# Kernel optimization log

Hardware: AMD Instinct MI355X
Metric: run time of the kernel (lower is better)

Reference implementation:

```python
import jax, jax.numpy as jnp
import numpy as np

HEAD_DIM = 64
AGGR = 4  # attn_aggr_ratio
BN_EPS = 1e-5


def _conv1x1(x, W, b=None):
    # x: [N, Cin, L], W: [Cout, Cin] -> [N, Cout, L]
    y = jnp.einsum('ncl,oc->nol', x, W)
    if b is not None:
        y = y + b[None, :, None]
    return y


def _bn(x, gamma, beta, mean, var):
    # BatchNorm1d, eval mode (running stats). x: [N, C, L]
    inv = gamma * jax.lax.rsqrt(var + BN_EPS)
    return x * inv[None, :, None] + (beta - mean * inv)[None, :, None]


def setup_inputs() -> dict:
    key = jax.random.key(0)
    ks = jax.random.split(key, 8)
    N, C, L = 4, 256, 4096
    s = 1.0 / np.sqrt(C)
    inp = {
        'x': jax.random.normal(ks[0], (N, C, L), jnp.float32),
        'Wq': jax.random.normal(ks[1], (C, C), jnp.float32) * s,
        'bq': jnp.zeros((C,), jnp.float32),
        'Wk': jax.random.normal(ks[2], (C, C), jnp.float32) * s,
        'bk': jnp.zeros((C,), jnp.float32),
        'Wv': jax.random.normal(ks[3], (C, C), jnp.float32) * s,
        'bv': jnp.zeros((C,), jnp.float32),
        'Wo': jax.random.normal(ks[4], (C, C), jnp.float32) * s,
        'bo': jnp.zeros((C,), jnp.float32),
        'Wa': jax.random.normal(ks[5], (C, C), jnp.float32) * s,
        'g1': jnp.ones((C,), jnp.float32), 'b1': jnp.zeros((C,), jnp.float32),
        'm1': jnp.zeros((C,), jnp.float32), 'v1': jnp.ones((C,), jnp.float32),
        'g2': jnp.ones((C,), jnp.float32), 'b2': jnp.zeros((C,), jnp.float32),
        'm2': jnp.zeros((C,), jnp.float32), 'v2': jnp.ones((C,), jnp.float32),
    }
    return inp


def reference(x, Wq, bq, Wk, bk, Wv, bv, Wo, bo, Wa,
              g1, b1, m1, v1, g2, b2, m2, v2):
    N, C, L = x.shape
    H, E = C // HEAD_DIM, HEAD_DIM
    # q projection on full-resolution input
    q = _conv1x1(x, Wq, bq).reshape(N, H, E, L)
    # LocalAwareAggregationBlock: avg+max pool (kernel=AGGR, L divisible), 1x1 conv, BN
    xp = x.reshape(N, C, L // AGGR, AGGR)
    xa = xp.mean(axis=-1) + xp.max(axis=-1)          # [N, C, L//AGGR]
    xa = _conv1x1(xa, Wa)                             # bias=False
    xa = _bn(xa, g1, b1, m1, v1)
    # post-aggregation norm
    xa = _bn(xa, g2, b2, m2, v2)
    k = _conv1x1(xa, Wk, bk).reshape(N, H, E, -1)     # [N, H, E, L2]
    v = _conv1x1(xa, Wv, bv).reshape(N, H, E, -1)
    # attention: softmax((q/sqrt(E))^T k) @ v^T
    scale = 1.0 / np.sqrt(E)
    scores = jnp.einsum('nhel,nhem->nhlm', q * scale, k)  # [N, H, L, L2]
    attn = jax.nn.softmax(scores, axis=-1)
    o = jnp.einsum('nhlm,nhem->nhel', attn, v).reshape(N, C, L)
    return _conv1x1(o, Wo, bo)
```

## Files before the change

### kernel.cpp

```cpp
#include <hip/hip_runtime.h>
#include <stdint.h>

constexpr int NBATCH = 4;
constexpr int CH     = 256;
constexpr int LEN    = 4096;
constexpr int LPOOL  = 1024;
constexpr int NH     = 4;
constexpr int HD     = 64;

typedef __attribute__((ext_vector_type(8))) short short8;
typedef __attribute__((ext_vector_type(4))) float float4e;
typedef __attribute__((ext_vector_type(16))) float float16e;
typedef __attribute__((ext_vector_type(2))) unsigned uint2v;

__device__ __forceinline__ unsigned short f2bf(float f) {
    union { unsigned int i; float f; } v; v.f = f;
    unsigned int lsb = (v.i >> 16) & 1u;
    v.i += 0x7fffu + lsb;
    return (unsigned short)(v.i >> 16);
}
__device__ __forceinline__ unsigned pack2bf(float lo, float hi) {
    unsigned a = __float_as_uint(lo) + 0x8000u;
    unsigned b = __float_as_uint(hi) + 0x8000u;
    return __builtin_amdgcn_perm(b, a, 0x07060302u);
}
__device__ __forceinline__ float fast_exp2(float x) {
#if __has_builtin(__builtin_amdgcn_exp2f)
    return __builtin_amdgcn_exp2f(x);
#else
    float r;
    asm("v_exp_f32 %0, %1" : "=v"(r) : "v"(x));
    return r;
#endif
}

__global__ __launch_bounds__(256) void transpool_setup(
    const float* __restrict__ x, unsigned short* __restrict__ xbf,
    unsigned short* __restrict__ poolT,
    const float* __restrict__ w0, const float* __restrict__ w1,
    const float* __restrict__ w2, const float* __restrict__ w3,
    const float* __restrict__ w4, unsigned short* __restrict__ outW,
    const float* __restrict__ g1, const float* __restrict__ b1,
    const float* __restrict__ m1, const float* __restrict__ v1,
    const float* __restrict__ g2, const float* __restrict__ b2,
    const float* __restrict__ m2, const float* __restrict__ v2,
    float* __restrict__ scale, float* __restrict__ shift,
    const float* __restrict__ bk, const float* __restrict__ bv,
    float* __restrict__ bkv)
{
    __shared__ float T[64][65];
    __shared__ float P16[64][17];
    int b = blockIdx.x, t = threadIdx.x;
    if (b >= 1024) {
        int sb = b - 1024;
        if (sb < 320) {
            int gid = sb * 256 + t;
            int w = gid >> 14;
            int off = (gid & 16383) * 4;
            const float* src = (w == 0) ? w0 : (w == 1) ? w1 : (w == 2) ? w2 : (w == 3) ? w3 : w4;
            float4 v = *(const float4*)(src + off);
            uint2 pk;
            pk.x = pack2bf(v.x, v.y);
            pk.y = pack2bf(v.z, v.w);
            *(uint2*)(outW + w * 65536 + off) = pk;
        } else {
            float inv1 = g1[t] * rsqrtf(v1[t] + 1e-5f);
            float inv2 = g2[t] * rsqrtf(v2[t] + 1e-5f);
            scale[t] = inv1 * inv2;
            shift[t] = (b1[t] - m1[t] * inv1) * inv2 + (b2[t] - m2[t] * inv2);
            bkv[t] = bk[t];
            bkv[256 + t] = bv[t];
        }
        return;
    }
    int n = b >> 8, c0 = ((b >> 6) & 3) * 64, l0 = (b & 63) * 64;
    const float* xp = x + ((size_t)n * CH + c0) * LEN + l0;
    #pragma unroll
    for (int i = 0; i < 4; i++) {
        int idx = t + i * 256;
        int c = idx >> 4, l4 = idx & 15;
        float4 v = *(const float4*)(xp + (size_t)c * LEN + l4 * 4);
        T[c][l4 * 4 + 0] = v.x; T[c][l4 * 4 + 1] = v.y;
        T[c][l4 * 4 + 2] = v.z; T[c][l4 * 4 + 3] = v.w;
        P16[c][l4] = (v.x + v.y + v.z + v.w) * 0.25f
                   + fmaxf(fmaxf(v.x, v.y), fmaxf(v.z, v.w));
    }
    __syncthreads();
    unsigned short* op = xbf + ((size_t)n * LEN + l0) * CH + c0;
    #pragma unroll
    for (int i = 0; i < 4; i++) {
        int idx = t + i * 256;
        int l = idx >> 4, c4 = idx & 15;
        uint2 pk;
        pk.x = pack2bf(T[c4 * 4 + 0][l], T[c4 * 4 + 1][l]);
        pk.y = pack2bf(T[c4 * 4 + 2][l], T[c4 * 4 + 3][l]);
        *(uint2*)(op + (size_t)l * CH + c4 * 4) = pk;
    }
    int p0 = l0 >> 2;
    #pragma unroll
    for (int k = 0; k < 2; k++) {
        int p = (t >> 5) + k * 8;
        int c2 = (t & 31) * 2;
        unsigned pk = pack2bf(P16[c2][p], P16[c2 + 1][p]);
        *(unsigned*)(poolT + ((size_t)n * LPOOL + p0 + p) * CH + c0 + c2) = pk;
    }
}

__global__ __launch_bounds__(256) void gemm_mfma(
    const unsigned short* __restrict__ A,
    const unsigned short* __restrict__ B, size_t bBatch,
    const float* __restrict__ biasRow,
    const float* __restrict__ scale, const float* __restrict__ shift,
    float* __restrict__ outF, size_t oFBatch,
    unsigned short* __restrict__ out1, size_t o1Batch, int cs1,
    unsigned short* __restrict__ out2, size_t o2Batch, int rs2, int rowSplit,
    int NN, float outScale)
{
    __shared__ unsigned short smem[2 * 128 * 72];
    unsigned short* As = smem;
    unsigned short* Bs = smem + 128 * 72;

    int n = blockIdx.z;
    int t = threadIdx.x;
    int wave = t >> 6, lane = t & 63, m = lane & 15, quad = lane >> 4;
    int wm = wave & 1, wn = wave >> 1;
    int rowTile = blockIdx.y * 128;
    int col0 = blockIdx.x * 128;

    const unsigned short* Ab = A + (size_t)rowTile * 256;
    const unsigned short* Bb = B + (size_t)n * bBatch + (size_t)col0 * 256;

    float4e acc[4][4] = {};

    for (int kk = 0; kk < 256; kk += 64) {
        #pragma unroll
        for (int i = 0; i < 4; i++) {
            int idx = t + i * 256;
            int row = idx >> 3, ch = idx & 7;
            *(uint4*)&As[row * 72 + ch * 8] = *(const uint4*)(Ab + (size_t)row * 256 + kk + ch * 8);
            *(uint4*)&Bs[row * 72 + ch * 8] = *(const uint4*)(Bb + (size_t)row * 256 + kk + ch * 8);
        }
        __syncthreads();
        #pragma unroll
        for (int kc = 0; kc < 2; kc++) {
            short8 af[4], bfr[4];
            #pragma unroll
            for (int i = 0; i < 4; i++)
                af[i] = *(const short8*)&As[(wm * 64 + i * 16 + m) * 72 + kc * 32 + quad * 8];
            #pragma unroll
            for (int j = 0; j < 4; j++)
                bfr[j] = *(const short8*)&Bs[(wn * 64 + j * 16 + m) * 72 + kc * 32 + quad * 8];
            #pragma unroll
            for (int i = 0; i < 4; i++)
                #pragma unroll
                for (int j = 0; j < 4; j++)
                    acc[i][j] = __builtin_amdgcn_mfma_f32_16x16x32_bf16(af[i], bfr[j], acc[i][j], 0, 0, 0);
        }
        __syncthreads();
    }

    if (outF) {
        float* TOf = (float*)smem;
        float* dst = outF + (size_t)n * oFBatch;
        #pragma unroll
        for (int half = 0; half < 2; half++) {
            __syncthreads();
            if (wm == half) {
                #pragma unroll
                for (int i = 0; i < 4; i++) {
                    int rowL = i * 16 + quad * 4;
                    int rowG = rowTile + half * 64 + rowL;
                    float br[4], sc[4], sh[4];
                    #pragma unroll
                    for (int r = 0; r < 4; r++) {
                        br[r] = biasRow ? biasRow[rowG + r] : 0.0f;
                        sc[r] = scale ? scale[rowG + r] : 1.0f;
                        sh[r] = shift ? shift[rowG + r] : 0.0f;
                    }
                    #pragma unroll
                    for (int j = 0; j < 4; j++) {
                        int colL = wn * 64 + j * 16 + m;
                        float4e c = acc[i][j];
                        #pragma unroll
                        for (int r = 0; r < 4; r++)
                            TOf[(rowL + r) * 128 + colL] = ((c[r] + br[r]) * sc[r] + sh[r]) * outScale;
                    }
                }
            }
            __syncthreads();
            #pragma unroll
            for (int w = 0; w < 8; w++) {
                int idx = t + w * 256;
                int row = idx >> 5, c4 = idx & 31;
                *(float4*)(dst + (size_t)(rowTile + half * 64 + row) * NN + col0 + c4 * 4) =
                    *(const float4*)&TOf[row * 128 + c4 * 4];
            }
        }
        return;
    }

    bool mode2 = (rowTile >= rowSplit);
    unsigned short* TO = smem;
    #pragma unroll
    for (int i = 0; i < 4; i++) {
        int rowL = wm * 64 + i * 16 + quad * 4;
        int rowG = rowTile + rowL;
        float br[4], sc[4], sh[4];
        #pragma unroll
        for (int r = 0; r < 4; r++) {
            br[r] = biasRow ? biasRow[rowG + r] : 0.0f;
            sc[r] = scale ? scale[rowG + r] : 1.0f;
            sh[r] = shift ? shift[rowG + r] : 0.0f;
        }
        #pragma unroll
        for (int j = 0; j < 4; j++) {
            int colL = wn * 64 + j * 16 + m;
            float4e c = acc[i][j];
            float v0 = ((c[0] + br[0]) * sc[0] + sh[0]) * outScale;
            float v1 = ((c[1] + br[1]) * sc[1] + sh[1]) * outScale;
            float v2 = ((c[2] + br[2]) * sc[2] + sh[2]) * outScale;
            float v3 = ((c[3] + br[3]) * sc[3] + sh[3]) * outScale;
            if (!mode2) {
                uint2 pk;
                pk.x = pack2bf(v0, v1);
                pk.y = pack2bf(v2, v3);
                *(uint2*)&TO[colL * 136 + rowL] = pk;
            } else {
                TO[(rowL + 0) * 136 + colL] = f2bf(v0);
                TO[(rowL + 1) * 136 + colL] = f2bf(v1);
                TO[(rowL + 2) * 136 + colL] = f2bf(v2);
                TO[(rowL + 3) * 136 + colL] = f2bf(v3);
            }
        }
    }
    __syncthreads();
    if (!mode2) {
        unsigned short* dst = out1 + (size_t)n * o1Batch;
        #pragma unroll
        for (int w = 0; w < 8; w++) {
            int idx = t + w * 256;
            int l = idx >> 4, ch = idx & 15;
            *(uint4*)(dst + (size_t)(col0 + l) * cs1 + rowTile + ch * 8) =
                *(const uint4*)&TO[l * 136 + ch * 8];
        }
    } else {
        unsigned short* dst = out2 + (size_t)n * o2Batch;
        int rowBase = rowTile - rowSplit;
        #pragma unroll
        for (int w = 0; w < 8; w++) {
            int idx = t + w * 256;
            int row = idx >> 4, ch = idx & 15;
            *(uint4*)(dst + (size_t)(rowBase + row) * rs2 + col0 + ch * 8) =
                *(const uint4*)&TO[row * 136 + ch * 8];
        }
    }
}

__global__ __launch_bounds__(256, 2) void attn_mfma(
    const unsigned short* __restrict__ Qb,
    const unsigned short* __restrict__ Kb,
    const unsigned short* __restrict__ Vb,
    unsigned short* __restrict__ Obf)
{
    __shared__ unsigned short Ks[2][64 * 64];
    __shared__ unsigned short Vs[2][64 * 64];

    int qb = blockIdx.x;
    int h  = blockIdx.y;
    int n  = blockIdx.z;
    int t  = threadIdx.x;
    int wave = t >> 6, lane = t & 63;
    int col = lane & 31;
    int hi  = lane >> 5;
    int l0 = qb * 128 + wave * 32;

    const unsigned short* qp = Qb + ((size_t)n * LEN + l0 + col) * CH + h * HD + hi * 8;
    short8 bQ[4];
    #pragma unroll
    for (int dc = 0; dc < 4; dc++)
        bQ[dc] = *(const short8*)(qp + dc * 16);

    float16e Oa[2];
    #pragma unroll
    for (int e = 0; e < 2; e++)
        #pragma unroll
        for (int r = 0; r < 16; r++) Oa[e][r] = 0.0f;
    float l_run = 0.0f;

    const unsigned short* KgBase = Kb + (size_t)n * LPOOL * CH + h * HD;
    const unsigned short* VgBase = Vb + ((size_t)n * CH + h * HD) * LPOOL;
    const float NEG = -17.312340f;

    int srow[2], sch[2], sdst[2];
    #pragma unroll
    for (int i = 0; i < 2; i++) {
        int idx = t + i * 256;
        srow[i] = idx >> 3; sch[i] = idx & 7;
        sdst[i] = srow[i] * 128 + ((sch[i] * 16) ^ ((srow[i] & 7) << 4));
    }
    const unsigned short* kp[2];
    const unsigned short* vp[2];
    #pragma unroll
    for (int i = 0; i < 2; i++) {
        kp[i] = KgBase + (size_t)srow[i] * CH + sch[i] * 8;
        vp[i] = VgBase + (size_t)srow[i] * LPOOL + sch[i] * 8;
    }
    int ldoff[2][4];
    #pragma unroll
    for (int g = 0; g < 2; g++)
        #pragma unroll
        for (int c = 0; c < 4; c++) {
            int row = g * 32 + col;
            ldoff[g][c] = row * 128 + ((c * 32 + hi * 16) ^ ((row & 7) << 4));
        }

    uint4 kreg[2], vreg[2];
    #pragma unroll
    for (int i = 0; i < 2; i++) {
        kreg[i] = *(const uint4*)kp[i];
        vreg[i] = *(const uint4*)vp[i];
        kp[i] += 64 * CH;
        vp[i] += 64;
    }
    #pragma unroll
    for (int i = 0; i < 2; i++) {
        *(uint4*)((char*)Ks[0] + sdst[i]) = kreg[i];
        *(uint4*)((char*)Vs[0] + sdst[i]) = vreg[i];
    }
    __syncthreads();

    for (int kt = 0; kt < 16; kt++) {
        int cur = kt & 1;
        if (kt < 15) {
            #pragma unroll
            for (int i = 0; i < 2; i++) {
                kreg[i] = *(const uint4*)kp[i];
                vreg[i] = *(const uint4*)vp[i];
                kp[i] += 64 * CH;
                vp[i] += 64;
            }
        }

        const char* KsC = (const char*)Ks[cur];
        const char* VsC = (const char*)Vs[cur];
        #pragma unroll
        for (int kh = 0; kh < 2; kh++) {
            float16e c;
            #pragma unroll
            for (int r = 0; r < 16; r++) c[r] = NEG;
            __builtin_amdgcn_s_setprio(1);
            #pragma unroll
            for (int dc = 0; dc < 4; dc++) {
                short8 a = *(const short8*)(KsC + ldoff[kh][dc]);
                c = __builtin_amdgcn_mfma_f32_32x32x16_bf16(a, bQ[dc], c, 0, 0, 0);
            }
            __builtin_amdgcn_s_setprio(0);
            float p[16];
            #pragma unroll
            for (int r = 0; r < 16; r++) p[r] = fast_exp2(c[r]);
            l_run += ((p[0] + p[1]) + (p[2] + p[3])) + ((p[4] + p[5]) + (p[6] + p[7]))
                   + ((p[8] + p[9]) + (p[10] + p[11])) + ((p[12] + p[13]) + (p[14] + p[15]));
            union { unsigned u[4]; short8 s; } bP[2];
            #pragma unroll
            for (int kc2 = 0; kc2 < 2; kc2++) {
                int rb = kc2 * 8;
                unsigned A0 = pack2bf(p[rb + 0], p[rb + 1]);
                unsigned B0 = pack2bf(p[rb + 4], p[rb + 5]);
                unsigned A1 = pack2bf(p[rb + 2], p[rb + 3]);
                unsigned B1 = pack2bf(p[rb + 6], p[rb + 7]);
                uint2v s0 = __builtin_amdgcn_permlane32_swap(A0, B0, false, false);
                uint2v s1 = __builtin_amdgcn_permlane32_swap(A1, B1, false, false);
                bP[kc2].u[0] = s0[0];
                bP[kc2].u[1] = s1[0];
                bP[kc2].u[2] = s0[1];
                bP[kc2].u[3] = s1[1];
            }
            __builtin_amdgcn_s_setprio(1);
            #pragma unroll
            for (int eh = 0; eh < 2; eh++)
                #pragma unroll
                for (int kc2 = 0; kc2 < 2; kc2++) {
                    short8 av = *(const short8*)(VsC + ldoff[eh][kh * 2 + kc2]);
                    Oa[eh] = __builtin_amdgcn_mfma_f32_32x32x16_bf16(av, bP[kc2].s, Oa[eh], 0, 0, 0);
                }
            __builtin_amdgcn_s_setprio(0);
        }

        if (kt < 15) {
            int nxt = cur ^ 1;
            #pragma unroll
            for (int i = 0; i < 2; i++) {
                *(uint4*)((char*)Ks[nxt] + sdst[i]) = kreg[i];
                *(uint4*)((char*)Vs[nxt] + sdst[i]) = vreg[i];
            }
            __syncthreads();
        }
    }

    float l = l_run + __shfl_xor(l_run, 32);
    float inv = 1.0f / l;
    unsigned short* op = Obf + ((size_t)n * LEN + l0 + col) * CH + h * HD + hi * 4;
    #pragma unroll
    for (int eh = 0; eh < 2; eh++)
        #pragma unroll
        for (int rq = 0; rq < 4; rq++) {
            int r = rq * 4;
            uint2 pk;
            pk.x = pack2bf(Oa[eh][r + 0] * inv, Oa[eh][r + 1] * inv);
            pk.y = pack2bf(Oa[eh][r + 2] * inv, Oa[eh][r + 3] * inv);
            *(uint2*)(op + eh * 32 + rq * 8) = pk;
        }
}

extern "C" void kernel_launch(void* const* d_in, const int* in_sizes, int n_in,
                              void* d_out, int out_size, void* d_ws, size_t ws_size,
                              hipStream_t stream)
{
    const float* x  = (const float*)d_in[0];
    const float* Wq = (const float*)d_in[1];
    const float* bq = (const float*)d_in[2];
    const float* Wk = (const float*)d_in[3];
    const float* bk = (const float*)d_in[4];
    const float* Wv = (const float*)d_in[5];
    const float* bv = (const float*)d_in[6];
    const float* Wo = (const float*)d_in[7];
    const float* bo = (const float*)d_in[8];
    const float* Wa = (const float*)d_in[9];
    const float* g1 = (const float*)d_in[10];
    const float* b1 = (const float*)d_in[11];
    const float* m1 = (const float*)d_in[12];
    const float* v1 = (const float*)d_in[13];
    const float* g2 = (const float*)d_in[14];
    const float* b2 = (const float*)d_in[15];
    const float* m2 = (const float*)d_in[16];
    const float* v2 = (const float*)d_in[17];

    float* wsf      = (float*)d_ws;
    float* bn_scale = wsf;
    float* bn_shift = wsf + 256;
    float* bkv      = wsf + 512;
    unsigned short* Wbf   = (unsigned short*)(wsf + 1024);
    unsigned short* xbf   = Wbf + 5 * 65536;
    unsigned short* poolT = xbf   + (size_t)NBATCH * LEN * CH;
    unsigned short* xabf  = poolT + (size_t)NBATCH * LPOOL * CH;
    unsigned short* Kbf   = xabf  + (size_t)NBATCH * LPOOL * CH;
    unsigned short* Vbf   = Kbf   + (size_t)NBATCH * LPOOL * CH;
    unsigned short* Qbf   = Vbf   + (size_t)NBATCH * LPOOL * CH;
    unsigned short* Obf   = Qbf   + (size_t)NBATCH * LEN * CH;

    transpool_setup<<<1345, 256, 0, stream>>>(x, xbf, poolT,
        Wq, Wk, Wv, Wo, Wa, Wbf,
        g1, b1, m1, v1, g2, b2, m2, v2, bn_scale, bn_shift, bk, bv, bkv);

    gemm_mfma<<<dim3(32, 2, 4), 256, 0, stream>>>(
        Wbf + 0 * 65536, xbf, (size_t)LEN * CH, bq, nullptr, nullptr,
        nullptr, 0, Qbf, (size_t)LEN * CH, 256, nullptr, 0, 0, 1 << 30,
        LEN, 0.18033688f);

    gemm_mfma<<<dim3(8, 2, 4), 256, 0, stream>>>(
        Wbf + 4 * 65536, poolT, (size_t)LPOOL * CH, nullptr, bn_scale, bn_shift,
        nullptr, 0, xabf, (size_t)LPOOL * CH, 256, nullptr, 0, 0, 1 << 30,
        LPOOL, 1.0f);

    gemm_mfma<<<dim3(8, 4, 4), 256, 0, stream>>>(
        Wbf + 1 * 65536, xabf, (size_t)LPOOL * CH, bkv, nullptr, nullptr,
        nullptr, 0, Kbf, (size_t)LPOOL * CH, 256, Vbf, (size_t)LPOOL * CH, LPOOL, 256,
        LPOOL, 1.0f);

    attn_mfma<<<dim3(LEN / 128, NH, NBATCH), 256, 0, stream>>>(Qbf, Kbf, Vbf, Obf);

    gemm_mfma<<<dim3(32, 2, 4), 256, 0, stream>>>(
        Wbf + 3 * 65536, Obf, (size_t)LEN * CH, bo, nullptr, nullptr,
        (float*)d_out, (size_t)CH * LEN, nullptr, 0, 0, nullptr, 0, 0, 1 << 30,
        LEN, 1.0f);
}
```

Baseline: 182.0 us.

## Split attention keys across waves and read K/V fragments directly from global

The attention kernel now gives each block 64 queries instead of 128. Within a block, two pairs of waves each cover half of the 1024 pooled keys, and their partial outputs and softmax sums are combined through shared memory at the end. The double-buffered LDS staging of K/V tiles and the per-tile barriers are gone: each lane loads its MFMA fragments straight from global/L2 memory, and launch bounds are raised to allow more resident blocks. The aim is more parallelism and occupancy with fewer syncs, at the cost of more, less coalesced global loads, since each K/V fragment is now fetched by twice as many blocks.

```diff
diff --git a/kernel.cpp b/kernel.cpp
--- a/kernel.cpp
+++ b/kernel.cpp
@@ -256,14 +256,13 @@
     }
 }
 
-__global__ __launch_bounds__(256, 2) void attn_mfma(
+__global__ __launch_bounds__(256, 4) void attn_mfma(
     const unsigned short* __restrict__ Qb,
     const unsigned short* __restrict__ Kb,
     const unsigned short* __restrict__ Vb,
     unsigned short* __restrict__ Obf)
 {
-    __shared__ unsigned short Ks[2][64 * 64];
-    __shared__ unsigned short Vs[2][64 * 64];
+    __shared__ float comb[2 * 64 * 33];
 
     int qb = blockIdx.x;
     int h  = blockIdx.y;
@@ -272,7 +271,10 @@
     int wave = t >> 6, lane = t & 63;
     int col = lane & 31;
     int hi  = lane >> 5;
-    int l0 = qb * 128 + wave * 32;
+    int qc = wave & 1;
+    int ks = wave >> 1;
+    int l0 = qb * 64 + qc * 32;
+    int kbase = ks * 512;
 
     const unsigned short* qp = Qb + ((size_t)n * LEN + l0 + col) * CH + h * HD + hi * 8;
     short8 bQ[4];
@@ -287,129 +289,101 @@
         for (int r = 0; r < 16; r++) Oa[e][r] = 0.0f;
     float l_run = 0.0f;
 
-    const unsigned short* KgBase = Kb + (size_t)n * LPOOL * CH + h * HD;
-    const unsigned short* VgBase = Vb + ((size_t)n * CH + h * HD) * LPOOL;
     const float NEG = -17.312340f;
 
-    int srow[2], sch[2], sdst[2];
-    #pragma unroll
-    for (int i = 0; i < 2; i++) {
-        int idx = t + i * 256;
-        srow[i] = idx >> 3; sch[i] = idx & 7;
-        sdst[i] = srow[i] * 128 + ((sch[i] * 16) ^ ((srow[i] & 7) << 4));
-    }
-    const unsigned short* kp[2];
-    const unsigned short* vp[2];
-    #pragma unroll
-    for (int i = 0; i < 2; i++) {
-        kp[i] = KgBase + (size_t)srow[i] * CH + sch[i] * 8;
-        vp[i] = VgBase + (size_t)srow[i] * LPOOL + sch[i] * 8;
-    }
-    int ldoff[2][4];
-    #pragma unroll
-    for (int g = 0; g < 2; g++)
-        #pragma unroll
-        for (int c = 0; c < 4; c++) {
-            int row = g * 32 + col;
-            ldoff[g][c] = row * 128 + ((c * 32 + hi * 16) ^ ((row & 7) << 4));
-        }
-
-    uint4 kreg[2], vreg[2];
-    #pragma unroll
-    for (int i = 0; i < 2; i++) {
-        kreg[i] = *(const uint4*)kp[i];
-        vreg[i] = *(const uint4*)vp[i];
-        kp[i] += 64 * CH;
-        vp[i] += 64;
-    }
-    #pragma unroll
-    for (int i = 0; i < 2; i++) {
-        *(uint4*)((char*)Ks[0] + sdst[i]) = kreg[i];
-        *(uint4*)((char*)Vs[0] + sdst[i]) = vreg[i];
+    const unsigned short* kPtr =
+        Kb + ((size_t)n * LPOOL + kbase + col) * CH + h * HD + hi * 8;
+    const unsigned short* vPtr0 =
+        Vb + ((size_t)n * CH + h * HD + col) * LPOOL + kbase + hi * 8;
+    const unsigned short* vPtr1 = vPtr0 + (size_t)32 * LPOOL;
+
+    #pragma unroll 2
+    for (int kt = 0; kt < 16; kt++) {
+        short8 kf0 = *(const short8*)(kPtr);
+        short8 kf1 = *(const short8*)(kPtr + 16);
+        short8 kf2 = *(const short8*)(kPtr + 32);
+        short8 kf3 = *(const short8*)(kPtr + 48);
+        short8 av00 = *(const short8*)(vPtr0);
+        short8 av01 = *(const short8*)(vPtr0 + 16);
+        short8 av10 = *(const short8*)(vPtr1);
+        short8 av11 = *(const short8*)(vPtr1 + 16);
+        kPtr  += 32 * CH;
+        vPtr0 += 32;
+        vPtr1 += 32;
+
+        float16e c;
+        #pragma unroll
+        for (int r = 0; r < 16; r++) c[r] = NEG;
+        __builtin_amdgcn_s_setprio(1);
+        c = __builtin_amdgcn_mfma_f32_32x32x16_bf16(kf0, bQ[0], c, 0, 0, 0);
+        c = __builtin_amdgcn_mfma_f32_32x32x16_bf16(kf1, bQ[1], c, 0, 0, 0);
+        c = __builtin_amdgcn_mfma_f32_32x32x16_bf16(kf2, bQ[2], c, 0, 0, 0);
+        c = __builtin_amdgcn_mfma_f32_32x32x16_bf16(kf3, bQ[3], c, 0, 0, 0);
+        __builtin_amdgcn_s_setprio(0);
+
+        float p[16];
+        #pragma unroll
+        for (int r = 0; r < 16; r++) p[r] = fast_exp2(c[r]);
+        l_run += ((p[0] + p[1]) + (p[2] + p[3])) + ((p[4] + p[5]) + (p[6] + p[7]))
+               + ((p[8] + p[9]) + (p[10] + p[11])) + ((p[12] + p[13]) + (p[14] + p[15]));
+
+        union { unsigned u[4]; short8 s; } bP[2];
+        #pragma unroll
+        for (int kc2 = 0; kc2 < 2; kc2++) {
+            int rb = kc2 * 8;
+            unsigned A0 = pack2bf(p[rb + 0], p[rb + 1]);
+            unsigned B0 = pack2bf(p[rb + 4], p[rb + 5]);
+            unsigned A1 = pack2bf(p[rb + 2], p[rb + 3]);
+            unsigned B1 = pack2bf(p[rb + 6], p[rb + 7]);
+            uint2v s0 = __builtin_amdgcn_permlane32_swap(A0, B0, false, false);
+            uint2v s1 = __builtin_amdgcn_permlane32_swap(A1, B1, false, false);
+            bP[kc2].u[0] = s0[0];
+            bP[kc2].u[1] = s1[0];
+            bP[kc2].u[2] = s0[1];
+            bP[kc2].u[3] = s1[1];
+        }
+
+        __builtin_amdgcn_s_setprio(1);
+        Oa[0] = __builtin_amdgcn_mfma_f32_32x32x16_bf16(av00, bP[0].s, Oa[0], 0, 0, 0);
+        Oa[0] = __builtin_amdgcn_mfma_f32_32x32x16_bf16(av01, bP[1].s, Oa[0], 0, 0, 0);
+        Oa[1] = __builtin_amdgcn_mfma_f32_32x32x16_bf16(av10, bP[0].s, Oa[1], 0, 0, 0);
+        Oa[1] = __builtin_amdgcn_mfma_f32_32x32x16_bf16(av11, bP[1].s, Oa[1], 0, 0, 0);
+        __builtin_amdgcn_s_setprio(0);
+    }
+
+    if (wave >= 2) {
+        float* cb = &comb[((wave - 2) * 64 + lane) * 33];
+        #pragma unroll
+        for (int eh = 0; eh < 2; eh++)
+            #pragma unroll
+            for (int r = 0; r < 16; r++)
+                cb[eh * 16 + r] = Oa[eh][r];
+        cb[32] = l_run;
     }
     __syncthreads();
-
-    for (int kt = 0; kt < 16; kt++) {
-        int cur = kt & 1;
-        if (kt < 15) {
-            #pragma unroll
-            for (int i = 0; i < 2; i++) {
-                kreg[i] = *(const uint4*)kp[i];
-                vreg[i] = *(const uint4*)vp[i];
-                kp[i] += 64 * CH;
-                vp[i] += 64;
+    if (wave < 2) {
+        const float* cb = &comb[(wave * 64 + lane) * 33];
+        #pragma unroll
+        for (int eh = 0; eh < 2; eh++)
+            #pragma unroll
+            for (int r = 0; r < 16; r++)
+                Oa[eh][r] += cb[eh * 16 + r];
+        l_run += cb[32];
+
+        float l = l_run + __shfl_xor(l_run, 32);
+        float inv = 1.0f / l;
+        unsigned short* op = Obf + ((size_t)n * LEN + l0 + col) * CH + h * HD + hi * 4;
+        #pragma unroll
+        for (int eh = 0; eh < 2; eh++)
+            #pragma unroll
+            for (int rq = 0; rq < 4; rq++) {
+                int r = rq * 4;
+                uint2 pk;
+                pk.x = pack2bf(Oa[eh][r + 0] * inv, Oa[eh][r + 1] * inv);
+                pk.y = pack2bf(Oa[eh][r + 2] * inv, Oa[eh][r + 3] * inv);
+                *(uint2*)(op + eh * 32 + rq * 8) = pk;
             }
-        }
-
-        const char* KsC = (const char*)Ks[cur];
-        const char* VsC = (const char*)Vs[cur];
-        #pragma unroll
-        for (int kh = 0; kh < 2; kh++) {
-            float16e c;
-            #pragma unroll
-            for (int r = 0; r < 16; r++) c[r] = NEG;
-            __builtin_amdgcn_s_setprio(1);
-            #pragma unroll
-            for (int dc = 0; dc < 4; dc++) {
-                short8 a = *(const short8*)(KsC + ldoff[kh][dc]);
-                c = __builtin_amdgcn_mfma_f32_32x32x16_bf16(a, bQ[dc], c, 0, 0, 0);
-            }
-            __builtin_amdgcn_s_setprio(0);
-            float p[16];
-            #pragma unroll
-            for (int r = 0; r < 16; r++) p[r] = fast_exp2(c[r]);
-            l_run += ((p[0] + p[1]) + (p[2] + p[3])) + ((p[4] + p[5]) + (p[6] + p[7]))
-                   + ((p[8] + p[9]) + (p[10] + p[11])) + ((p[12] + p[13]) + (p[14] + p[15]));
-            union { unsigned u[4]; short8 s; } bP[2];
-            #pragma unroll
-            for (int kc2 = 0; kc2 < 2; kc2++) {
-                int rb = kc2 * 8;
-                unsigned A0 = pack2bf(p[rb + 0], p[rb + 1]);
-                unsigned B0 = pack2bf(p[rb + 4], p[rb + 5]);
-                unsigned A1 = pack2bf(p[rb + 2], p[rb + 3]);
-                unsigned B1 = pack2bf(p[rb + 6], p[rb + 7]);
-                uint2v s0 = __builtin_amdgcn_permlane32_swap(A0, B0, false, false);
-                uint2v s1 = __builtin_amdgcn_permlane32_swap(A1, B1, false, false);
-                bP[kc2].u[0] = s0[0];
-                bP[kc2].u[1] = s1[0];
-                bP[kc2].u[2] = s0[1];
-                bP[kc2].u[3] = s1[1];
-            }
-            __builtin_amdgcn_s_setprio(1);
-            #pragma unroll
-            for (int eh = 0; eh < 2; eh++)
-                #pragma unroll
-                for (int kc2 = 0; kc2 < 2; kc2++) {
-                    short8 av = *(const short8*)(VsC + ldoff[eh][kh * 2 + kc2]);
-                    Oa[eh] = __builtin_amdgcn_mfma_f32_32x32x16_bf16(av, bP[kc2].s, Oa[eh], 0, 0, 0);
-                }
-            __builtin_amdgcn_s_setprio(0);
-        }
-
-        if (kt < 15) {
-            int nxt = cur ^ 1;
-            #pragma unroll
-            for (int i = 0; i < 2; i++) {
-                *(uint4*)((char*)Ks[nxt] + sdst[i]) = kreg[i];
-                *(uint4*)((char*)Vs[nxt] + sdst[i]) = vreg[i];
-            }
-            __syncthreads();
-        }
-    }
-
-    float l = l_run + __shfl_xor(l_run, 32);
-    float inv = 1.0f / l;
-    unsigned short* op = Obf + ((size_t)n * LEN + l0 + col) * CH + h * HD + hi * 4;
-    #pragma unroll
-    for (int eh = 0; eh < 2; eh++)
-        #pragma unroll
-        for (int rq = 0; rq < 4; rq++) {
-            int r = rq * 4;
-            uint2 pk;
-            pk.x = pack2bf(Oa[eh][r + 0] * inv, Oa[eh][r + 1] * inv);
-            pk.y = pack2bf(Oa[eh][r + 2] * inv, Oa[eh][r + 3] * inv);
-            *(uint2*)(op + eh * 32 + rq * 8) = pk;
-        }
+    }
 }
 
 extern "C" void kernel_launch(void* const* d_in, const int* in_sizes, int n_in,
@@ -467,7 +441,7 @@
         nullptr, 0, Kbf, (size_t)LPOOL * CH, 256, Vbf, (size_t)LPOOL * CH, LPOOL, 256,
         LPOOL, 1.0f);
 
-    attn_mfma<<<dim3(LEN / 128, NH, NBATCH), 256, 0, stream>>>(Qbf, Kbf, Vbf, Obf);
+    attn_mfma<<<dim3(LEN / 64, NH, NBATCH), 256, 0, stream>>>(Qbf, Kbf, Vbf, Obf);
 
     gemm_mfma<<<dim3(32, 2, 4), 256, 0, stream>>>(
         Wbf + 3 * 65536, Obf, (size_t)LEN * CH, bo, nullptr, nullptr,
```

Result: slower. 201.6 us (+10.7%).
